# Kernel tuning notes

Hardware: AMD Instinct MI355X
Metric: run time of the kernel (lower is better)

Reference implementation:

```python
import jax, jax.numpy as jnp
import numpy as np

DIM = 256
HEADS = 8
SEQ = 4096
SCALE = DIM ** -0.5  # note: original scales by full dim, not head dim


def setup_inputs() -> dict:
    key = jax.random.key(0)
    ks = jax.random.split(key, 5)
    x = jax.random.normal(ks[0], (SEQ, DIM), dtype=jnp.float32)
    w_qkv = jax.random.normal(ks[1], (DIM, 3 * DIM), dtype=jnp.float32) * (DIM ** -0.5)
    b_qkv = jnp.zeros((3 * DIM,), dtype=jnp.float32)
    w_out = jax.random.normal(ks[2], (DIM, DIM), dtype=jnp.float32) * (DIM ** -0.5)
    b_out = jnp.zeros((DIM,), dtype=jnp.float32)
    return {"x": x, "w_qkv": w_qkv, "b_qkv": b_qkv, "w_out": w_out, "b_out": b_out}


def reference(x, w_qkv, b_qkv, w_out, b_out):
    n, dim = x.shape
    h = HEADS
    d = dim // h
    qkv = x @ w_qkv + b_qkv                      # [n, 3*dim]
    q, k, v = jnp.split(qkv, 3, axis=-1)         # each [n, dim]
    # 'n (h d) -> h n d'
    q = q.reshape(n, h, d).transpose(1, 0, 2)
    k = k.reshape(n, h, d).transpose(1, 0, 2)
    v = v.reshape(n, h, d).transpose(1, 0, 2)
    dots = jnp.einsum('hid,hjd->hij', q, k) * SCALE  # [h, n, n]
    attn = jax.nn.softmax(dots, axis=-1)
    out = jnp.einsum('hij,hjd->hid', attn, v)        # [h, n, d]
    out = out.transpose(1, 0, 2).reshape(n, dim)     # 'h n d -> n (h d)'
    return out @ w_out + b_out                       # [n, dim]
```

## Files before the change

kernel.cpp:

```cpp
#include <hip/hip_runtime.h>
#include <stdint.h>

#define SEQ   4096
#define DIM   256
#define HDIM  32
#define HEADS 8
#define W3    768
#define LOG2E 1.4426950408889634f

typedef float  f32x4  __attribute__((ext_vector_type(4)));
typedef float  fl4    __attribute__((ext_vector_type(4)));
typedef short  bf16x8 __attribute__((ext_vector_type(8)));
typedef short  bf16x4 __attribute__((ext_vector_type(4)));

static __device__ __forceinline__ f32x4 MFMA_PV(bf16x4 a, bf16x4 b, f32x4 c) {
#if defined(__HIP_DEVICE_COMPILE__)
# if __has_builtin(__builtin_amdgcn_mfma_f32_16x16x16_bf16)
    return __builtin_amdgcn_mfma_f32_16x16x16_bf16(a, b, c, 0, 0, 0);
# elif __has_builtin(__builtin_amdgcn_mfma_f32_16x16x16bf16_1k)
    return __builtin_amdgcn_mfma_f32_16x16x16bf16_1k(a, b, c, 0, 0, 0);
# else
    f32x4 d;
    asm volatile("v_mfma_f32_16x16x16_bf16 %0, %1, %2, %3"
                 : "=v"(d) : "v"(a), "v"(b), "v"(c));
    return d;
# endif
#else
    (void)a; (void)b;
    return c;
#endif
}

__device__ __forceinline__ unsigned short f2bf(float f) {
    union { __bf16 h; unsigned short u; } v;
    v.h = (__bf16)f;
    return v.u;
}
__device__ __forceinline__ short f2bf_s(float f) {
    union { __bf16 h; short s; } v;
    v.h = (__bf16)f;
    return v.s;
}

__global__ __launch_bounds__(256) void prep_kernel(
    const float* __restrict__ x, const float* __restrict__ wqkv,
    const float* __restrict__ wout,
    unsigned short* __restrict__ xb,
    unsigned short* __restrict__ wt,
    unsigned short* __restrict__ wot)
{
    __shared__ float lds[64][65];
    const int b   = blockIdx.x;
    const int tid = threadIdx.x;
    if (b < 64) {
        const float* src;
        unsigned short* dst;
        int N, i0, j0;
        if (b < 48) {
            src = wqkv; dst = wt; N = W3;
            i0 = (b & 3) * 64; j0 = (b >> 2) * 64;
        } else {
            int bb = b - 48;
            src = wout; dst = wot; N = DIM;
            i0 = (bb & 3) * 64; j0 = (bb >> 2) * 64;
        }
        const int c = tid & 63, grp = tid >> 6;
        #pragma unroll
        for (int k = 0; k < 16; ++k) {
            int r = grp * 16 + k;
            lds[r][c] = src[(size_t)(i0 + r) * N + j0 + c];
        }
        __syncthreads();
        #pragma unroll
        for (int k = 0; k < 16; ++k) {
            int cc = grp * 16 + k;
            dst[(size_t)(j0 + cc) * DIM + i0 + c] = f2bf(lds[c][cc]);
        }
    } else {
        const fl4* __restrict__ x4 = (const fl4*)x;
        const int total4 = SEQ * DIM / 4;
        for (int i = (b - 64) * 256 + tid; i < total4; i += 64 * 256) {
            fl4 v = x4[i];
            ushort4 o;
            o.x = f2bf(v[0]); o.y = f2bf(v[1]);
            o.z = f2bf(v[2]); o.w = f2bf(v[3]);
            *reinterpret_cast<ushort4*>(xb + (size_t)i * 4) = o;
        }
    }
}

__global__ __launch_bounds__(256) void qkv_gemm(
    const unsigned short* __restrict__ xb,
    const unsigned short* __restrict__ wt,
    const float* __restrict__ bqkv,
    unsigned short* __restrict__ Qb,
    unsigned short* __restrict__ Kb,
    unsigned short* __restrict__ Vb)
{
    const int wid  = threadIdx.x >> 6;
    const int lane = threadIdx.x & 63;
    const int g    = lane >> 4, li = lane & 15;
    const int row0 = blockIdx.x * 64 + wid * 16;
    const int col0 = blockIdx.y * 64;

    f32x4 acc[4];
    #pragma unroll
    for (int c = 0; c < 4; ++c)
        acc[c] = (f32x4){0.f, 0.f, 0.f, 0.f};

    #pragma unroll
    for (int ks = 0; ks < DIM; ks += 32) {
        bf16x8 a = *(const bf16x8*)(xb + (size_t)(row0 + li) * DIM + ks + g * 8);
        bf16x8 b[4];
        #pragma unroll
        for (int c = 0; c < 4; ++c)
            b[c] = *(const bf16x8*)(wt + (size_t)(col0 + 16 * c + li) * DIM + ks + g * 8);
        #pragma unroll
        for (int c = 0; c < 4; ++c)
            acc[c] = __builtin_amdgcn_mfma_f32_16x16x32_bf16(a, b[c], acc[c], 0, 0, 0);
    }

    #pragma unroll
    for (int c = 0; c < 4; ++c)
        #pragma unroll
        for (int r = 0; r < 4; ++r) {
            int row = row0 + g * 4 + r;
            int col = col0 + 16 * c + li;
            float v = acc[c][r] + bqkv[col];
            int sec = col >> 8;
            int cc  = col & 255;
            int hh  = cc >> 5, dd = cc & 31;
            if (sec == 0)
                Qb[((size_t)hh * SEQ + row) * HDIM + dd] = f2bf(v * (0.0625f * LOG2E));
            else if (sec == 1)
                Kb[((size_t)hh * SEQ + row) * HDIM + dd] = f2bf(v);
            else
                Vb[(size_t)hh * SEQ * HDIM + ((size_t)(row >> 4) * HDIM + dd) * 16 + (row & 15)] = f2bf(v);
        }
}

__global__ __launch_bounds__(256) void attn_kernel(
    const unsigned short* __restrict__ Qb,
    const unsigned short* __restrict__ Kb,
    const unsigned short* __restrict__ Vb,
    float* __restrict__ Opart,
    float* __restrict__ Lp,
    int nc)
{
    __shared__ float obuf[2][16 * 64];
    __shared__ float lbuf[2][2 * 64];
    const int wid  = threadIdx.x >> 6;
    const int lane = threadIdx.x & 63;
    const int g    = lane >> 4, li = lane & 15;
    const int head = blockIdx.y;
    const int chunk = blockIdx.z;
    const int qs   = wid & 1;
    const int half = wid >> 1;
    const int r0   = blockIdx.x * 64 + qs * 32;
    const int span  = SEQ / nc;
    const int wspan = span >> 1;
    const int jb0   = chunk * span + half * wspan;
    const int ntile = wspan / 64;

    const unsigned short* Qh = Qb + (size_t)head * SEQ * HDIM;
    const unsigned short* kp = Kb + (size_t)head * SEQ * HDIM + (size_t)jb0 * HDIM
                             + (size_t)li * HDIM + g * 8;
    const unsigned short* vp = Vb + (size_t)head * SEQ * HDIM + (size_t)jb0 * HDIM
                             + (size_t)li * 16 + 4 * g;

    bf16x8 aq[2];
    #pragma unroll
    for (int t = 0; t < 2; ++t)
        aq[t] = *(const bf16x8*)(Qh + (size_t)(r0 + 16 * t + li) * HDIM + g * 8);

    f32x4 o[2][2];
    #pragma unroll
    for (int t = 0; t < 2; ++t)
        #pragma unroll
        for (int nt = 0; nt < 2; ++nt)
            o[t][nt] = (f32x4){0.f, 0.f, 0.f, 0.f};
    float lacc[2] = {0.f, 0.f};

    const f32x4 zero4 = (f32x4){0.f, 0.f, 0.f, 0.f};

#define LOADK(DST, P) do {                                                    \
    _Pragma("unroll")                                                         \
    for (int c_ = 0; c_ < 4; ++c_)                                            \
        DST[c_] = *(const bf16x8*)((P) + c_ * (16 * HDIM));                   \
} while (0)

#define TILE(BK, VP) do {                                                     \
    bf16x4 bv_[4][2];                                                         \
    _Pragma("unroll")                                                         \
    for (int c_ = 0; c_ < 4; ++c_)                                            \
        _Pragma("unroll")                                                     \
        for (int nt_ = 0; nt_ < 2; ++nt_)                                     \
            bv_[c_][nt_] = *(const bf16x4*)((VP) + c_ * (16 * HDIM) + nt_ * 256); \
    bf16x4 pa_[2][4];                                                         \
    _Pragma("unroll")                                                         \
    for (int t_ = 0; t_ < 2; ++t_) {                                          \
        f32x4 s_[4];                                                          \
        _Pragma("unroll")                                                     \
        for (int c_ = 0; c_ < 4; ++c_)                                        \
            s_[c_] = __builtin_amdgcn_mfma_f32_16x16x32_bf16(BK[c_], aq[t_], zero4, 0, 0, 0); \
        _Pragma("unroll")                                                     \
        for (int c_ = 0; c_ < 4; ++c_) {                                      \
            float p0_ = __builtin_amdgcn_exp2f(s_[c_][0]);                    \
            float p1_ = __builtin_amdgcn_exp2f(s_[c_][1]);                    \
            float p2_ = __builtin_amdgcn_exp2f(s_[c_][2]);                    \
            float p3_ = __builtin_amdgcn_exp2f(s_[c_][3]);                    \
            lacc[t_] += (p0_ + p1_) + (p2_ + p3_);                            \
            bf16x4 f_;                                                        \
            f_[0] = f2bf_s(p0_); f_[1] = f2bf_s(p1_);                         \
            f_[2] = f2bf_s(p2_); f_[3] = f2bf_s(p3_);                         \
            pa_[t_][c_] = f_;                                                 \
        }                                                                     \
    }                                                                         \
    _Pragma("unroll")                                                         \
    for (int c_ = 0; c_ < 4; ++c_)                                            \
        _Pragma("unroll")                                                     \
        for (int t_ = 0; t_ < 2; ++t_)                                        \
            _Pragma("unroll")                                                 \
            for (int nt_ = 0; nt_ < 2; ++nt_)                                 \
                o[t_][nt_] = MFMA_PV(pa_[t_][c_], bv_[c_][nt_], o[t_][nt_]);  \
} while (0)

    bf16x8 bkA[4], bkB[4];
    LOADK(bkA, kp);
    for (int i = 0; i < ntile - 2; i += 2) {
        LOADK(bkB, kp + 2048);
        TILE(bkA, vp);
        LOADK(bkA, kp + 4096);
        TILE(bkB, vp + 2048);
        kp += 4096; vp += 4096;
    }
    LOADK(bkB, kp + 2048);
    TILE(bkA, vp);
    TILE(bkB, vp + 2048);
#undef LOADK
#undef TILE

    if (half == 1) {
        #pragma unroll
        for (int t = 0; t < 2; ++t)
            #pragma unroll
            for (int nt = 0; nt < 2; ++nt)
                #pragma unroll
                for (int r = 0; r < 4; ++r)
                    obuf[qs][((t * 2 + nt) * 4 + r) * 64 + lane] = o[t][nt][r];
        #pragma unroll
        for (int t = 0; t < 2; ++t)
            lbuf[qs][t * 64 + lane] = lacc[t];
    }
    __syncthreads();
    if (half == 1) return;

    #pragma unroll
    for (int t = 0; t < 2; ++t)
        #pragma unroll
        for (int nt = 0; nt < 2; ++nt)
            #pragma unroll
            for (int r = 0; r < 4; ++r)
                o[t][nt][r] += obuf[qs][((t * 2 + nt) * 4 + r) * 64 + lane];
    #pragma unroll
    for (int t = 0; t < 2; ++t)
        lacc[t] += lbuf[qs][t * 64 + lane];

    #pragma unroll
    for (int t = 0; t < 2; ++t) {
        float L = lacc[t];
        L += __shfl_xor(L, 16);
        L += __shfl_xor(L, 32);
        lacc[t] = L;
    }

    float* Oc = Opart + (size_t)chunk * SEQ * DIM;
    #pragma unroll
    for (int t = 0; t < 2; ++t)
        #pragma unroll
        for (int nt = 0; nt < 2; ++nt)
            #pragma unroll
            for (int r = 0; r < 4; ++r) {
                int row = r0 + 16 * t + g * 4 + r;
                int col = head * HDIM + 16 * nt + li;
                Oc[(size_t)row * DIM + col] = o[t][nt][r];
            }
    if (lane < 16) {
        #pragma unroll
        for (int t = 0; t < 2; ++t) {
            int row = r0 + 16 * t + lane;
            Lp[((size_t)chunk * HEADS + head) * SEQ + row] = lacc[t];
        }
    }
}

__global__ __launch_bounds__(256) void combine_kernel(
    const float* __restrict__ Opart, const float* __restrict__ Lp,
    unsigned short* __restrict__ AO, int nc)
{
    int idx = blockIdx.x * 256 + threadIdx.x;
    int row = idx >> 6;
    int cp  = (idx & 63) << 2;
    int head = cp >> 5;
    float L = 0.f;
    fl4 a = (fl4){0.f, 0.f, 0.f, 0.f};
    for (int i = 0; i < nc; ++i) {
        L += Lp[((size_t)i * HEADS + head) * SEQ + row];
        a += *(const fl4*)(Opart + (size_t)i * SEQ * DIM + (size_t)row * DIM + cp);
    }
    float inv = 1.f / L;
    ushort4 pk;
    pk.x = f2bf(a[0] * inv); pk.y = f2bf(a[1] * inv);
    pk.z = f2bf(a[2] * inv); pk.w = f2bf(a[3] * inv);
    *reinterpret_cast<ushort4*>(AO + (size_t)row * DIM + cp) = pk;
}

__global__ __launch_bounds__(256) void out_gemm(
    const unsigned short* __restrict__ AO,
    const unsigned short* __restrict__ wot,
    const float* __restrict__ bout,
    float* __restrict__ out)
{
    const int wid  = threadIdx.x >> 6;
    const int lane = threadIdx.x & 63;
    const int g    = lane >> 4, li = lane & 15;
    const int row0 = blockIdx.x * 64 + wid * 16;
    const int col0 = blockIdx.y * 64;

    f32x4 acc[4];
    #pragma unroll
    for (int c = 0; c < 4; ++c)
        acc[c] = (f32x4){0.f, 0.f, 0.f, 0.f};

    #pragma unroll
    for (int ks = 0; ks < DIM; ks += 32) {
        bf16x8 a = *(const bf16x8*)(AO + (size_t)(row0 + li) * DIM + ks + g * 8);
        bf16x8 b[4];
        #pragma unroll
        for (int c = 0; c < 4; ++c)
            b[c] = *(const bf16x8*)(wot + (size_t)(col0 + 16 * c + li) * DIM + ks + g * 8);
        #pragma unroll
        for (int c = 0; c < 4; ++c)
            acc[c] = __builtin_amdgcn_mfma_f32_16x16x32_bf16(a, b[c], acc[c], 0, 0, 0);
    }

    #pragma unroll
    for (int c = 0; c < 4; ++c)
        #pragma unroll
        for (int r = 0; r < 4; ++r) {
            int row = row0 + g * 4 + r;
            int col = col0 + 16 * c + li;
            out[(size_t)row * DIM + col] = acc[c][r] + bout[col];
        }
}

extern "C" void kernel_launch(void* const* d_in, const int* in_sizes, int n_in,
                              void* d_out, int out_size, void* d_ws, size_t ws_size,
                              hipStream_t stream)
{
    const float* x    = (const float*)d_in[0];
    const float* wqkv = (const float*)d_in[1];
    const float* bqkv = (const float*)d_in[2];
    const float* wout = (const float*)d_in[3];
    const float* bout = (const float*)d_in[4];
    float* out = (float*)d_out;

    char* ws = (char*)d_ws;
    const size_t OFF_XB  = 0;
    const size_t OFF_WT  = 2097152;
    const size_t OFF_WOT = 2490368;
    const size_t OFF_QB  = 2621440;
    const size_t OFF_KB  = 4718592;
    const size_t OFF_VT  = 6815744;
    const size_t OFF_AO  = 8912896;
    const size_t OFF_OP  = 11010048;
    const size_t OP_CH   = (size_t)SEQ * DIM * 4;
    const size_t LP_CH   = (size_t)HEADS * SEQ * 4;

    int nc = 4;
    while (nc > 1 && OFF_OP + (size_t)nc * (OP_CH + LP_CH) > ws_size) nc >>= 1;
    if (OFF_OP + (size_t)nc * (OP_CH + LP_CH) > ws_size) return;

    unsigned short* xb  = (unsigned short*)(ws + OFF_XB);
    unsigned short* wt  = (unsigned short*)(ws + OFF_WT);
    unsigned short* wot = (unsigned short*)(ws + OFF_WOT);
    unsigned short* Qb  = (unsigned short*)(ws + OFF_QB);
    unsigned short* Kb  = (unsigned short*)(ws + OFF_KB);
    unsigned short* Vb  = (unsigned short*)(ws + OFF_VT);
    unsigned short* AO  = (unsigned short*)(ws + OFF_AO);
    float* Opart = (float*)(ws + OFF_OP);
    float* Lp    = (float*)(ws + OFF_OP + (size_t)nc * OP_CH);

    hipLaunchKernelGGL(prep_kernel, dim3(128), dim3(256), 0, stream,
                       x, wqkv, wout, xb, wt, wot);
    hipLaunchKernelGGL(qkv_gemm, dim3(64, 12), dim3(256), 0, stream,
                       xb, wt, bqkv, Qb, Kb, Vb);
    hipLaunchKernelGGL(attn_kernel, dim3(SEQ / 64, HEADS, nc), dim3(256), 0, stream,
                       Qb, Kb, Vb, Opart, Lp, nc);
    hipLaunchKernelGGL(combine_kernel, dim3(SEQ * DIM / 1024), dim3(256), 0, stream,
                       Opart, Lp, AO, nc);
    hipLaunchKernelGGL(out_gemm, dim3(SEQ / 64, DIM / 64), dim3(256), 0, stream,
                       AO, wot, bout, out);
}
```

Measured before the change: 75.77 us.

## Interleave QK and PV MFMAs per column chunk, drop K double-buffering, raise occupancy

```diff
diff --git a/kernel.cpp b/kernel.cpp
--- a/kernel.cpp
+++ b/kernel.cpp
@@ -9,6 +9,7 @@
 #define LOG2E 1.4426950408889634f
 
 typedef float  f32x4  __attribute__((ext_vector_type(4)));
+typedef float  f32x2  __attribute__((ext_vector_type(2)));
 typedef float  fl4    __attribute__((ext_vector_type(4)));
 typedef short  bf16x8 __attribute__((ext_vector_type(8)));
 typedef short  bf16x4 __attribute__((ext_vector_type(4)));
@@ -139,7 +140,7 @@
         }
 }
 
-__global__ __launch_bounds__(256) void attn_kernel(
+__global__ __launch_bounds__(256, 8) void attn_kernel(
     const unsigned short* __restrict__ Qb,
     const unsigned short* __restrict__ Kb,
     const unsigned short* __restrict__ Vb,
@@ -179,66 +180,57 @@
         #pragma unroll
         for (int nt = 0; nt < 2; ++nt)
             o[t][nt] = (f32x4){0.f, 0.f, 0.f, 0.f};
-    float lacc[2] = {0.f, 0.f};
+    f32x2 lacc2[2];
+    lacc2[0] = (f32x2){0.f, 0.f};
+    lacc2[1] = (f32x2){0.f, 0.f};
 
     const f32x4 zero4 = (f32x4){0.f, 0.f, 0.f, 0.f};
 
-#define LOADK(DST, P) do {                                                    \
-    _Pragma("unroll")                                                         \
-    for (int c_ = 0; c_ < 4; ++c_)                                            \
-        DST[c_] = *(const bf16x8*)((P) + c_ * (16 * HDIM));                   \
-} while (0)
-
-#define TILE(BK, VP) do {                                                     \
-    bf16x4 bv_[4][2];                                                         \
-    _Pragma("unroll")                                                         \
-    for (int c_ = 0; c_ < 4; ++c_)                                            \
-        _Pragma("unroll")                                                     \
-        for (int nt_ = 0; nt_ < 2; ++nt_)                                     \
-            bv_[c_][nt_] = *(const bf16x4*)((VP) + c_ * (16 * HDIM) + nt_ * 256); \
-    bf16x4 pa_[2][4];                                                         \
-    _Pragma("unroll")                                                         \
-    for (int t_ = 0; t_ < 2; ++t_) {                                          \
-        f32x4 s_[4];                                                          \
-        _Pragma("unroll")                                                     \
-        for (int c_ = 0; c_ < 4; ++c_)                                        \
-            s_[c_] = __builtin_amdgcn_mfma_f32_16x16x32_bf16(BK[c_], aq[t_], zero4, 0, 0, 0); \
-        _Pragma("unroll")                                                     \
-        for (int c_ = 0; c_ < 4; ++c_) {                                      \
-            float p0_ = __builtin_amdgcn_exp2f(s_[c_][0]);                    \
-            float p1_ = __builtin_amdgcn_exp2f(s_[c_][1]);                    \
-            float p2_ = __builtin_amdgcn_exp2f(s_[c_][2]);                    \
-            float p3_ = __builtin_amdgcn_exp2f(s_[c_][3]);                    \
-            lacc[t_] += (p0_ + p1_) + (p2_ + p3_);                            \
-            bf16x4 f_;                                                        \
-            f_[0] = f2bf_s(p0_); f_[1] = f2bf_s(p1_);                         \
-            f_[2] = f2bf_s(p2_); f_[3] = f2bf_s(p3_);                         \
-            pa_[t_][c_] = f_;                                                 \
-        }                                                                     \
-    }                                                                         \
-    _Pragma("unroll")                                                         \
-    for (int c_ = 0; c_ < 4; ++c_)                                            \
-        _Pragma("unroll")                                                     \
-        for (int t_ = 0; t_ < 2; ++t_)                                        \
-            _Pragma("unroll")                                                 \
-            for (int nt_ = 0; nt_ < 2; ++nt_)                                 \
-                o[t_][nt_] = MFMA_PV(pa_[t_][c_], bv_[c_][nt_], o[t_][nt_]);  \
-} while (0)
-
-    bf16x8 bkA[4], bkB[4];
-    LOADK(bkA, kp);
-    for (int i = 0; i < ntile - 2; i += 2) {
-        LOADK(bkB, kp + 2048);
-        TILE(bkA, vp);
-        LOADK(bkA, kp + 4096);
-        TILE(bkB, vp + 2048);
-        kp += 4096; vp += 4096;
-    }
-    LOADK(bkB, kp + 2048);
-    TILE(bkA, vp);
-    TILE(bkB, vp + 2048);
-#undef LOADK
-#undef TILE
+    for (int it = 0; it < ntile; ++it) {
+        bf16x8 bk[4];
+        #pragma unroll
+        for (int c = 0; c < 4; ++c)
+            bk[c] = *(const bf16x8*)(kp + c * (16 * HDIM));
+        bf16x4 bv[4][2];
+        #pragma unroll
+        for (int c = 0; c < 4; ++c)
+            #pragma unroll
+            for (int nt = 0; nt < 2; ++nt)
+                bv[c][nt] = *(const bf16x4*)(vp + c * (16 * HDIM) + nt * 256);
+
+        #pragma unroll
+        for (int c = 0; c < 4; ++c) {
+            f32x4 s0 = __builtin_amdgcn_mfma_f32_16x16x32_bf16(bk[c], aq[0], zero4, 0, 0, 0);
+            f32x4 s1 = __builtin_amdgcn_mfma_f32_16x16x32_bf16(bk[c], aq[1], zero4, 0, 0, 0);
+            {
+                float p0 = __builtin_amdgcn_exp2f(s0[0]);
+                float p1 = __builtin_amdgcn_exp2f(s0[1]);
+                float p2 = __builtin_amdgcn_exp2f(s0[2]);
+                float p3 = __builtin_amdgcn_exp2f(s0[3]);
+                f32x2 ps; ps[0] = p0 + p2; ps[1] = p1 + p3;
+                lacc2[0] += ps;
+                bf16x4 pa;
+                pa[0] = f2bf_s(p0); pa[1] = f2bf_s(p1);
+                pa[2] = f2bf_s(p2); pa[3] = f2bf_s(p3);
+                o[0][0] = MFMA_PV(pa, bv[c][0], o[0][0]);
+                o[0][1] = MFMA_PV(pa, bv[c][1], o[0][1]);
+            }
+            {
+                float p0 = __builtin_amdgcn_exp2f(s1[0]);
+                float p1 = __builtin_amdgcn_exp2f(s1[1]);
+                float p2 = __builtin_amdgcn_exp2f(s1[2]);
+                float p3 = __builtin_amdgcn_exp2f(s1[3]);
+                f32x2 ps; ps[0] = p0 + p2; ps[1] = p1 + p3;
+                lacc2[1] += ps;
+                bf16x4 pa;
+                pa[0] = f2bf_s(p0); pa[1] = f2bf_s(p1);
+                pa[2] = f2bf_s(p2); pa[3] = f2bf_s(p3);
+                o[1][0] = MFMA_PV(pa, bv[c][0], o[1][0]);
+                o[1][1] = MFMA_PV(pa, bv[c][1], o[1][1]);
+            }
+        }
+        kp += 2048; vp += 2048;
+    }
 
     if (half == 1) {
         #pragma unroll
@@ -250,21 +242,21 @@
                     obuf[qs][((t * 2 + nt) * 4 + r) * 64 + lane] = o[t][nt][r];
         #pragma unroll
         for (int t = 0; t < 2; ++t)
-            lbuf[qs][t * 64 + lane] = lacc[t];
+            lbuf[qs][t * 64 + lane] = lacc2[t][0] + lacc2[t][1];
     }
     __syncthreads();
     if (half == 1) return;
 
-    #pragma unroll
-    for (int t = 0; t < 2; ++t)
+    float lacc[2];
+    #pragma unroll
+    for (int t = 0; t < 2; ++t) {
         #pragma unroll
         for (int nt = 0; nt < 2; ++nt)
             #pragma unroll
             for (int r = 0; r < 4; ++r)
                 o[t][nt][r] += obuf[qs][((t * 2 + nt) * 4 + r) * 64 + lane];
-    #pragma unroll
-    for (int t = 0; t < 2; ++t)
-        lacc[t] += lbuf[qs][t * 64 + lane];
+        lacc[t] = lacc2[t][0] + lacc2[t][1] + lbuf[qs][t * 64 + lane];
+    }
 
     #pragma unroll
     for (int t = 0; t < 2; ++t) {
```

New measurement: 124.0 us. 63.6% more time.
